# Kernel optimization log

Measured on AMD Instinct MI355X. Metric: run time of the kernel, lower is better.

## Reference

```python
import jax, jax.numpy as jnp
import numpy as np

B, S, D = 4, 2048, 1024
H = 16
HD = D // H  # head_dim = 64


def setup_inputs() -> dict:
    key = jax.random.key(0)
    ks = jax.random.split(key, 8)
    scale = 1.0 / np.sqrt(D)
    return {
        "X_Q": jax.random.normal(ks[0], (B, S, D), dtype=jnp.float32),
        "X_KV": jax.random.normal(ks[1], (B, S, D), dtype=jnp.float32),
        # q_proj: Linear(D, D), weights stored as (in, out)
        "q_w": jax.random.normal(ks[2], (D, D), dtype=jnp.float32) * scale,
        "q_b": jax.random.normal(ks[3], (D,), dtype=jnp.float32) * scale,
        # kv_proj: Linear(D, 2*D)
        "kv_w": jax.random.normal(ks[4], (D, 2 * D), dtype=jnp.float32) * scale,
        "kv_b": jax.random.normal(ks[5], (2 * D,), dtype=jnp.float32) * scale,
        # out_proj: Linear(D, D) (query_dim == input_dim)
        "out_w": jax.random.normal(ks[6], (D, D), dtype=jnp.float32) * scale,
        "out_b": jax.random.normal(ks[7], (D,), dtype=jnp.float32) * scale,
    }


def reference(X_Q, X_KV, q_w, q_b, kv_w, kv_b, out_w, out_b):
    # projections
    q = X_Q @ q_w + q_b                      # [b, s, D]
    kv = X_KV @ kv_w + kv_b                  # [b, l, 2D]
    k, v = jnp.split(kv, 2, axis=-1)         # each [b, l, D]

    def split_heads(t):
        b, m, _ = t.shape
        return t.reshape(b, m, H, HD).transpose(0, 2, 1, 3)  # [b, h, m, d]

    q, k, v = split_heads(q), split_heads(k), split_heads(v)

    # standard attention: full SxL scores (non-flash path)
    scores = jnp.einsum("bhsd,bhld->bhsl", q, k) / np.sqrt(HD)
    attn = jax.nn.softmax(scores, axis=-1)   # dropout_p = 0 -> identity
    out = jnp.einsum("bhsl,bhld->bhsd", attn, v)

    # merge heads: [b, h, s, d] -> [b, s, h*d]
    out = out.transpose(0, 2, 1, 3).reshape(B, S, D)
    return out @ out_w + out_b
```

## Files before the change

kernel.cpp:

```cpp
#include <hip/hip_runtime.h>
#include <hip/hip_bf16.h>
#include <math.h>

#define B_  4
#define S_  2048
#define D_  1024
#define H_  16
#define HD_ 64

typedef __bf16 bf16;
typedef __bf16 bf16x4 __attribute__((ext_vector_type(4)));
typedef __bf16 bf16x8 __attribute__((ext_vector_type(8)));
typedef float  floatx4 __attribute__((ext_vector_type(4)));

#define QSCALE 0.18033688011112042f

__device__ __forceinline__ void async_load16(const bf16* g, bf16* l) {
  __builtin_amdgcn_global_load_lds(
      (const __attribute__((address_space(1))) void*)g,
      (__attribute__((address_space(3))) void*)l, 16, 0, 0);
}

__global__ __launch_bounds__(256) void cast_both(
    const float* __restrict__ ina, bf16* __restrict__ outa,
    const float* __restrict__ inb, bf16* __restrict__ outb) {
  int bid = blockIdx.x;
  const float* in;
  bf16* out;
  int i;
  if (bid < 8192) { in = ina; out = outa; i = (bid * 256 + threadIdx.x) * 4; }
  else            { in = inb; out = outb; i = ((bid - 8192) * 256 + threadIdx.x) * 4; }
  float4 v = *reinterpret_cast<const float4*>(in + i);
  bf16x4 o;
  o[0] = (bf16)v.x; o[1] = (bf16)v.y; o[2] = (bf16)v.z; o[3] = (bf16)v.w;
  *reinterpret_cast<bf16x4*>(out + i) = o;
}

__global__ __launch_bounds__(256) void transcast_all(
    const float* __restrict__ qw, bf16* __restrict__ qwT,
    const float* __restrict__ kvw, bf16* __restrict__ kvwT,
    const float* __restrict__ ow, bf16* __restrict__ owT) {
  __shared__ float tile[32][33];
  int bid = blockIdx.x;
  const float* in; bf16* out; int N, lb;
  if (bid < 1024)      { in = qw;  out = qwT;  N = 1024; lb = bid; }
  else if (bid < 3072) { in = kvw; out = kvwT; N = 2048; lb = bid - 1024; }
  else                 { in = ow;  out = owT;  N = 1024; lb = bid - 3072; }
  int nx = N >> 5;
  int n0 = (lb % nx) * 32, k0 = (lb / nx) * 32;
  int tx = threadIdx.x & 31, ty = threadIdx.x >> 5;
  #pragma unroll
  for (int i = ty; i < 32; i += 8)
    tile[i][tx] = in[(size_t)(k0 + i) * N + n0 + tx];
  __syncthreads();
  #pragma unroll
  for (int i = ty; i < 32; i += 8)
    out[(size_t)(n0 + i) * 1024 + k0 + tx] = (bf16)tile[tx][i];
}

template <int MODE>
__device__ __forceinline__ void gemm_body(
    const bf16* __restrict__ A, const bf16* __restrict__ Bt,
    const float* __restrict__ bias, void* __restrict__ out,
    int M, int N, int K, int bx, int by,
    bf16 (*As)[64], bf16 (*Bs)[64]) {
  const int tid  = threadIdx.x;
  const int m0   = by * 128;
  const int n0   = bx * 128;
  const int w    = tid >> 6;
  const int lane = tid & 63;
  const int lr   = lane & 15;
  const int lq   = lane >> 4;
  const int wm   = (w >> 1) * 64;
  const int wn   = (w & 1) * 64;

  const int srow = lane >> 3;
  const int sg   = (lane & 7) ^ srow;
  const bf16* aptr = A  + (size_t)(m0 + 32 * w + srow) * K + 8 * sg;
  const bf16* bptr = Bt + (size_t)(n0 + 32 * w + srow) * K + 8 * sg;

  floatx4 acc[4][4];
  #pragma unroll
  for (int i = 0; i < 4; i++)
    #pragma unroll
    for (int j = 0; j < 4; j++)
      acc[i][j] = floatx4{0.f, 0.f, 0.f, 0.f};

  for (int k0 = 0; k0 < K; k0 += 64) {
    __syncthreads();
    #pragma unroll
    for (int p = 0; p < 4; p++) {
      async_load16(aptr + (size_t)8 * p * K + k0, &As[32 * w + 8 * p][0]);
      async_load16(bptr + (size_t)8 * p * K + k0, &Bs[32 * w + 8 * p][0]);
    }
    __syncthreads();
    #pragma unroll
    for (int kc = 0; kc < 2; kc++) {
      const int sw = 8 * ((kc * 4 + lq) ^ (lr & 7));
      bf16x8 af[4], bfv[4];
      #pragma unroll
      for (int t = 0; t < 4; t++)
        af[t] = *reinterpret_cast<const bf16x8*>(&As[wm + 16 * t + lr][sw]);
      #pragma unroll
      for (int t = 0; t < 4; t++)
        bfv[t] = *reinterpret_cast<const bf16x8*>(&Bs[wn + 16 * t + lr][sw]);
      #pragma unroll
      for (int i = 0; i < 4; i++)
        #pragma unroll
        for (int j = 0; j < 4; j++)
          acc[i][j] = __builtin_amdgcn_mfma_f32_16x16x32_bf16(af[i], bfv[j], acc[i][j], 0, 0, 0);
    }
  }

  #pragma unroll
  for (int i = 0; i < 4; i++) {
    int row_base = m0 + wm + 16 * i + lq * 4;
    #pragma unroll
    for (int j = 0; j < 4; j++) {
      int col = n0 + wn + 16 * j + lr;
      float bv = bias[col];
      if (MODE == 2 && col >= 1024) {
        int b = row_base >> 11, s0 = row_base & 2047;
        int c = col - 1024, h = c >> 6, d = c & 63;
        bf16* Vt = (bf16*)out + (size_t)B_ * H_ * S_ * HD_;
        bf16x4 pk;
        #pragma unroll
        for (int r = 0; r < 4; r++) pk[r] = (bf16)(acc[i][j][r] + bv);
        *reinterpret_cast<bf16x4*>(
            &Vt[(((size_t)b * H_ + h) * HD_ + d) * S_ + s0]) = pk;
        continue;
      }
      #pragma unroll
      for (int r = 0; r < 4; r++) {
        int row = row_base + r;
        float v = acc[i][j][r] + bv;
        if (MODE == 0) {
          ((float*)out)[(size_t)row * N + col] = v;
        } else if (MODE == 1) {
          int b = row >> 11, s = row & 2047;
          int h = col >> 6, d = col & 63;
          ((bf16*)out)[(((size_t)b * H_ + h) * S_ + s) * HD_ + d] =
              (bf16)(v * QSCALE);
        } else {
          int b = row >> 11, s = row & 2047;
          int h = col >> 6, d = col & 63;
          ((bf16*)out)[(((size_t)b * H_ + h) * S_ + s) * HD_ + d] = (bf16)v;
        }
      }
    }
  }
}

__global__ __launch_bounds__(256) void gemm_out(
    const bf16* __restrict__ A, const bf16* __restrict__ Bt,
    const float* __restrict__ bias, void* __restrict__ out,
    int M, int N, int K) {
  __shared__ bf16 As[128][64];
  __shared__ bf16 Bs[128][64];
  gemm_body<0>(A, Bt, bias, out, M, N, K, blockIdx.x, blockIdx.y, As, Bs);
}

__global__ __launch_bounds__(256) void gemm_qkv(
    const bf16* __restrict__ Xq, const bf16* __restrict__ qwT,
    const float* __restrict__ q_b, bf16* __restrict__ Qb,
    const bf16* __restrict__ Xkv, const bf16* __restrict__ kvwT,
    const float* __restrict__ kv_b, bf16* __restrict__ KVb) {
  __shared__ bf16 As[128][64];
  __shared__ bf16 Bs[128][64];
  int bid = blockIdx.x;
  if (bid < 512) {
    gemm_body<1>(Xq, qwT, q_b, Qb, 8192, 1024, 1024, bid & 7, bid >> 3, As, Bs);
  } else {
    int b2 = bid - 512;
    gemm_body<2>(Xkv, kvwT, kv_b, KVb, 8192, 2048, 1024, b2 & 15, b2 >> 4, As, Bs);
  }
}

__global__ __launch_bounds__(512, 2) void attn_kernel(
    const bf16* __restrict__ Q, const bf16* __restrict__ Kb,
    const bf16* __restrict__ Vt, bf16* __restrict__ out) {
  __shared__ bf16 smem[32768];

  const int tid  = threadIdx.x;
  const int w    = tid >> 6;
  const int lane = tid & 63;
  const int lr   = lane & 15;
  const int lq   = lane >> 4;
  const int bh   = blockIdx.x;
  const int q0   = blockIdx.y * 512;
  const size_t base = (size_t)bh * S_ * HD_;

  bf16* pw = smem + 16384 + w * 2048;

  const int srow = lane >> 3;
  const int sg   = (lane & 7) ^ srow;

  const bf16* kptr = Kb + base + (size_t)(8 * w + srow) * HD_ + 8 * sg;
  const bf16* vptr = Vt + base + (size_t)(8 * w + srow) * S_  + 8 * sg;

  async_load16(kptr, smem + 8 * w * 64);
  async_load16(vptr, smem + 4096 + 8 * w * 64);

  bf16x8 bq[4][2];
  #pragma unroll
  for (int g = 0; g < 4; g++) {
    const bf16* qrow = Q + base + (size_t)(q0 + 64 * w + 16 * g + lr) * HD_;
    bq[g][0] = *reinterpret_cast<const bf16x8*>(qrow + lq * 8);
    bq[g][1] = *reinterpret_cast<const bf16x8*>(qrow + 32 + lq * 8);
  }

  const int sw0 = 8 * ((0 + lq) ^ (lr & 7));
  const int sw1 = 8 * ((4 + lq) ^ (lr & 7));
  const int plx = lr >> 1;

  float l_i[4] = {0.f, 0.f, 0.f, 0.f};
  floatx4 o_acc[4][4];
  #pragma unroll
  for (int g = 0; g < 4; g++)
    #pragma unroll
    for (int t = 0; t < 4; t++) o_acc[g][t] = floatx4{0.f, 0.f, 0.f, 0.f};

  __syncthreads();

  const bf16* kpf = kptr + (size_t)64 * HD_;
  const bf16* vpf = vptr + 64;

  const int NIT = S_ / 64;
  for (int it = 0; it < NIT; it++) {
    bf16* ks  = smem + (it & 1) * 8192;
    bf16* vts = ks + 4096;

    if (it + 1 < NIT) {
      bf16* ksn = smem + ((it + 1) & 1) * 8192;
      async_load16(kpf, ksn + 8 * w * 64);
      async_load16(vpf, ksn + 4096 + 8 * w * 64);
    }

    auto qkt = [&](int t) {
      bf16x8 ak0 = *reinterpret_cast<const bf16x8*>(ks + (16 * t + lr) * 64 + sw0);
      bf16x8 ak1 = *reinterpret_cast<const bf16x8*>(ks + (16 * t + lr) * 64 + sw1);
      floatx4 sc[4];
      #pragma unroll
      for (int g = 0; g < 4; g++) {
        sc[g] = __builtin_amdgcn_mfma_f32_16x16x32_bf16(ak0, bq[g][0],
                    floatx4{0.f, 0.f, 0.f, 0.f}, 0, 0, 0);
        sc[g] = __builtin_amdgcn_mfma_f32_16x16x32_bf16(ak1, bq[g][1], sc[g], 0, 0, 0);
      }
      const int pcol = 4 * ((4 * (t & 1) + lq) ^ plx);
      #pragma unroll
      for (int g = 0; g < 4; g++) {
        bf16x4 pk;
        float lsum = 0.f;
        #pragma unroll
        for (int r = 0; r < 4; r++) {
          float p = __builtin_amdgcn_exp2f(sc[g][r]);
          lsum += p;
          pk[r] = (bf16)p;
        }
        l_i[g] += lsum;
        *reinterpret_cast<bf16x4*>(&pw[(16 * g + lr) * 32 + pcol]) = pk;
      }
    };

    auto pv = [&](int sw) {
      bf16x8 bp[4];
      #pragma unroll
      for (int g = 0; g < 4; g++) {
        union { bf16x4 h[2]; bf16x8 v; } f;
        f.h[0] = *reinterpret_cast<const bf16x4*>(
            &pw[(16 * g + lr) * 32 + 4 * ((2 * lq + 0) ^ plx)]);
        f.h[1] = *reinterpret_cast<const bf16x4*>(
            &pw[(16 * g + lr) * 32 + 4 * ((2 * lq + 1) ^ plx)]);
        bp[g] = f.v;
      }
      __builtin_amdgcn_s_setprio(1);
      #pragma unroll
      for (int t2 = 0; t2 < 4; t2++) {
        bf16x8 av = *reinterpret_cast<const bf16x8*>(vts + (16 * t2 + lr) * 64 + sw);
        #pragma unroll
        for (int g = 0; g < 4; g++)
          o_acc[g][t2] = __builtin_amdgcn_mfma_f32_16x16x32_bf16(av, bp[g], o_acc[g][t2], 0, 0, 0);
      }
      __builtin_amdgcn_s_setprio(0);
    };

    qkt(0);
    qkt(1);
    __builtin_amdgcn_wave_barrier();
    pv(sw0);
    __builtin_amdgcn_wave_barrier();
    qkt(2);
    qkt(3);
    __builtin_amdgcn_wave_barrier();
    pv(sw1);

    kpf += (size_t)64 * HD_;
    vpf += 64;
    __syncthreads();
  }

  #pragma unroll
  for (int g = 0; g < 4; g++) {
    l_i[g] += __shfl_xor(l_i[g], 16, 64);
    l_i[g] += __shfl_xor(l_i[g], 32, 64);
  }

  const int b = bh >> 4, h = bh & 15;
  #pragma unroll
  for (int g = 0; g < 4; g++) {
    const float inv = 1.0f / l_i[g];
    const int qrow = q0 + 64 * w + 16 * g + lr;
    bf16* orow = out + ((size_t)b * S_ + qrow) * D_ + h * HD_;
    #pragma unroll
    for (int t = 0; t < 4; t++) {
      bf16x4 pk;
      #pragma unroll
      for (int r = 0; r < 4; r++) pk[r] = (bf16)(o_acc[g][t][r] * inv);
      *reinterpret_cast<bf16x4*>(&orow[16 * t + lq * 4]) = pk;
    }
  }
}

extern "C" void kernel_launch(void* const* d_in, const int* in_sizes, int n_in,
                              void* d_out, int out_size, void* d_ws, size_t ws_size,
                              hipStream_t stream) {
  const float* X_Q   = (const float*)d_in[0];
  const float* X_KV  = (const float*)d_in[1];
  const float* q_w   = (const float*)d_in[2];
  const float* q_b   = (const float*)d_in[3];
  const float* kv_w  = (const float*)d_in[4];
  const float* kv_b  = (const float*)d_in[5];
  const float* out_w = (const float*)d_in[6];
  const float* out_b = (const float*)d_in[7];
  float* out = (float*)d_out;

  char* ws = (char*)d_ws;
  const size_t MB = 1024 * 1024;
  bf16* Xq   = (bf16*)(ws + 0);
  bf16* Xkv  = (bf16*)(ws + 16 * MB);
  bf16* Qb   = (bf16*)(ws + 32 * MB);
  bf16* Kb   = (bf16*)(ws + 48 * MB);
  bf16* qwT  = (bf16*)(ws + 80 * MB);
  bf16* kvwT = (bf16*)(ws + 82 * MB);
  bf16* owT  = (bf16*)(ws + 86 * MB);
  bf16* Vt   = Kb + (size_t)B_ * H_ * S_ * HD_;
  bf16* attn = Xq;

  cast_both<<<16384, 256, 0, stream>>>(X_Q, Xq, X_KV, Xkv);
  transcast_all<<<4096, 256, 0, stream>>>(q_w, qwT, kv_w, kvwT, out_w, owT);

  gemm_qkv<<<1536, 256, 0, stream>>>(Xq, qwT, q_b, Qb, Xkv, kvwT, kv_b, Kb);
  attn_kernel<<<dim3(64, 4), 512, 0, stream>>>(Qb, Kb, Vt, attn);
  gemm_out<<<dim3(8, 64), 256, 0, stream>>>(attn, owT, out_b, out, 8192, 1024, 1024);
}
```

Baseline: 305.7 us.

## Load K/V fragments directly from global in attention, shrink blocks, fuse prep kernels

Result: slower. 343.7 us (+12.5%).

```diff
diff --git a/kernel.cpp b/kernel.cpp
--- a/kernel.cpp
+++ b/kernel.cpp
@@ -21,27 +21,25 @@
       (__attribute__((address_space(3))) void*)l, 16, 0, 0);
 }
 
-__global__ __launch_bounds__(256) void cast_both(
-    const float* __restrict__ ina, bf16* __restrict__ outa,
-    const float* __restrict__ inb, bf16* __restrict__ outb) {
-  int bid = blockIdx.x;
-  const float* in;
-  bf16* out;
-  int i;
-  if (bid < 8192) { in = ina; out = outa; i = (bid * 256 + threadIdx.x) * 4; }
-  else            { in = inb; out = outb; i = ((bid - 8192) * 256 + threadIdx.x) * 4; }
-  float4 v = *reinterpret_cast<const float4*>(in + i);
-  bf16x4 o;
-  o[0] = (bf16)v.x; o[1] = (bf16)v.y; o[2] = (bf16)v.z; o[3] = (bf16)v.w;
-  *reinterpret_cast<bf16x4*>(out + i) = o;
-}
-
-__global__ __launch_bounds__(256) void transcast_all(
+__global__ __launch_bounds__(256) void prep_all(
+    const float* __restrict__ xa, bf16* __restrict__ oa,
+    const float* __restrict__ xb, bf16* __restrict__ ob,
     const float* __restrict__ qw, bf16* __restrict__ qwT,
     const float* __restrict__ kvw, bf16* __restrict__ kvwT,
     const float* __restrict__ ow, bf16* __restrict__ owT) {
   __shared__ float tile[32][33];
   int bid = blockIdx.x;
+  if (bid < 16384) {
+    const float* in; bf16* out; int i;
+    if (bid < 8192) { in = xa; out = oa; i = (bid * 256 + threadIdx.x) * 4; }
+    else            { in = xb; out = ob; i = ((bid - 8192) * 256 + threadIdx.x) * 4; }
+    float4 v = *reinterpret_cast<const float4*>(in + i);
+    bf16x4 o;
+    o[0] = (bf16)v.x; o[1] = (bf16)v.y; o[2] = (bf16)v.z; o[3] = (bf16)v.w;
+    *reinterpret_cast<bf16x4*>(out + i) = o;
+    return;
+  }
+  bid -= 16384;
   const float* in; bf16* out; int N, lb;
   if (bid < 1024)      { in = qw;  out = qwT;  N = 1024; lb = bid; }
   else if (bid < 3072) { in = kvw; out = kvwT; N = 2048; lb = bid - 1024; }
@@ -176,10 +174,10 @@
   }
 }
 
-__global__ __launch_bounds__(512, 2) void attn_kernel(
+__global__ __launch_bounds__(256, 2) void attn_kernel(
     const bf16* __restrict__ Q, const bf16* __restrict__ Kb,
     const bf16* __restrict__ Vt, bf16* __restrict__ out) {
-  __shared__ bf16 smem[32768];
+  __shared__ bf16 smem[8192];
 
   const int tid  = threadIdx.x;
   const int w    = tid >> 6;
@@ -187,19 +185,13 @@
   const int lr   = lane & 15;
   const int lq   = lane >> 4;
   const int bh   = blockIdx.x;
-  const int q0   = blockIdx.y * 512;
+  const int q0   = blockIdx.y * 256;
   const size_t base = (size_t)bh * S_ * HD_;
 
-  bf16* pw = smem + 16384 + w * 2048;
-
-  const int srow = lane >> 3;
-  const int sg   = (lane & 7) ^ srow;
-
-  const bf16* kptr = Kb + base + (size_t)(8 * w + srow) * HD_ + 8 * sg;
-  const bf16* vptr = Vt + base + (size_t)(8 * w + srow) * S_  + 8 * sg;
-
-  async_load16(kptr, smem + 8 * w * 64);
-  async_load16(vptr, smem + 4096 + 8 * w * 64);
+  bf16* pw = smem + w * 2048;
+
+  const bf16* kit = Kb + base + (size_t)lr * HD_ + 8 * lq;
+  const bf16* vit = Vt + base + (size_t)lr * S_ + 8 * lq;
 
   bf16x8 bq[4][2];
   #pragma unroll
@@ -209,8 +201,6 @@
     bq[g][1] = *reinterpret_cast<const bf16x8*>(qrow + 32 + lq * 8);
   }
 
-  const int sw0 = 8 * ((0 + lq) ^ (lr & 7));
-  const int sw1 = 8 * ((4 + lq) ^ (lr & 7));
   const int plx = lr >> 1;
 
   float l_i[4] = {0.f, 0.f, 0.f, 0.f};
@@ -220,25 +210,11 @@
     #pragma unroll
     for (int t = 0; t < 4; t++) o_acc[g][t] = floatx4{0.f, 0.f, 0.f, 0.f};
 
-  __syncthreads();
-
-  const bf16* kpf = kptr + (size_t)64 * HD_;
-  const bf16* vpf = vptr + 64;
-
   const int NIT = S_ / 64;
   for (int it = 0; it < NIT; it++) {
-    bf16* ks  = smem + (it & 1) * 8192;
-    bf16* vts = ks + 4096;
-
-    if (it + 1 < NIT) {
-      bf16* ksn = smem + ((it + 1) & 1) * 8192;
-      async_load16(kpf, ksn + 8 * w * 64);
-      async_load16(vpf, ksn + 4096 + 8 * w * 64);
-    }
-
     auto qkt = [&](int t) {
-      bf16x8 ak0 = *reinterpret_cast<const bf16x8*>(ks + (16 * t + lr) * 64 + sw0);
-      bf16x8 ak1 = *reinterpret_cast<const bf16x8*>(ks + (16 * t + lr) * 64 + sw1);
+      bf16x8 ak0 = *reinterpret_cast<const bf16x8*>(kit + 16 * t * HD_);
+      bf16x8 ak1 = *reinterpret_cast<const bf16x8*>(kit + 16 * t * HD_ + 32);
       floatx4 sc[4];
       #pragma unroll
       for (int g = 0; g < 4; g++) {
@@ -262,7 +238,7 @@
       }
     };
 
-    auto pv = [&](int sw) {
+    auto pv = [&](const bf16x8* av) {
       bf16x8 bp[4];
       #pragma unroll
       for (int g = 0; g < 4; g++) {
@@ -275,28 +251,33 @@
       }
       __builtin_amdgcn_s_setprio(1);
       #pragma unroll
-      for (int t2 = 0; t2 < 4; t2++) {
-        bf16x8 av = *reinterpret_cast<const bf16x8*>(vts + (16 * t2 + lr) * 64 + sw);
+      for (int t2 = 0; t2 < 4; t2++)
         #pragma unroll
         for (int g = 0; g < 4; g++)
-          o_acc[g][t2] = __builtin_amdgcn_mfma_f32_16x16x32_bf16(av, bp[g], o_acc[g][t2], 0, 0, 0);
-      }
+          o_acc[g][t2] = __builtin_amdgcn_mfma_f32_16x16x32_bf16(av[t2], bp[g], o_acc[g][t2], 0, 0, 0);
       __builtin_amdgcn_s_setprio(0);
     };
 
+    bf16x8 av0[4];
+    #pragma unroll
+    for (int t2 = 0; t2 < 4; t2++)
+      av0[t2] = *reinterpret_cast<const bf16x8*>(vit + (size_t)16 * t2 * S_);
     qkt(0);
     qkt(1);
     __builtin_amdgcn_wave_barrier();
-    pv(sw0);
+    pv(av0);
     __builtin_amdgcn_wave_barrier();
+    bf16x8 av1[4];
+    #pragma unroll
+    for (int t2 = 0; t2 < 4; t2++)
+      av1[t2] = *reinterpret_cast<const bf16x8*>(vit + (size_t)16 * t2 * S_ + 32);
     qkt(2);
     qkt(3);
     __builtin_amdgcn_wave_barrier();
-    pv(sw1);
-
-    kpf += (size_t)64 * HD_;
-    vpf += 64;
-    __syncthreads();
+    pv(av1);
+
+    kit += 64 * HD_;
+    vit += 64;
   }
 
   #pragma unroll
@@ -346,10 +327,9 @@
   bf16* Vt   = Kb + (size_t)B_ * H_ * S_ * HD_;
   bf16* attn = Xq;
 
-  cast_both<<<16384, 256, 0, stream>>>(X_Q, Xq, X_KV, Xkv);
-  transcast_all<<<4096, 256, 0, stream>>>(q_w, qwT, kv_w, kvwT, out_w, owT);
-
+  prep_all<<<20480, 256, 0, stream>>>(X_Q, Xq, X_KV, Xkv,
+                                      q_w, qwT, kv_w, kvwT, out_w, owT);
   gemm_qkv<<<1536, 256, 0, stream>>>(Xq, qwT, q_b, Qb, Xkv, kvwT, kv_b, Kb);
-  attn_kernel<<<dim3(64, 4), 512, 0, stream>>>(Qb, Kb, Vt, attn);
+  attn_kernel<<<dim3(64, 8), 256, 0, stream>>>(Qb, Kb, Vt, attn);
   gemm_out<<<dim3(8, 64), 256, 0, stream>>>(attn, owT, out_b, out, 8192, 1024, 1024);
 }
```
